# Performance work log

Measured on AMD Instinct MI355X. Metric: run time of the kernel, lower is better.

## Reference

```python
import jax, jax.numpy as jnp
import numpy as np

B, T, D, H = 2, 2048, 1024, 16
DH = D // H

def setup_inputs() -> dict:
    key = jax.random.key(0)
    ks = jax.random.split(key, 5)
    scale = 1.0 / np.sqrt(D)
    x = jax.random.normal(ks[0], (B, T, D), dtype=jnp.float32)
    Wq = jax.random.normal(ks[1], (D, D), dtype=jnp.float32) * scale
    Wk = jax.random.normal(ks[2], (D, D), dtype=jnp.float32) * scale
    Wv = jax.random.normal(ks[3], (D, D), dtype=jnp.float32) * scale
    Wo = jax.random.normal(ks[4], (D, D), dtype=jnp.float32) * scale
    # causal mask: True means masked (matches torch masked_fill semantics)
    mask = jnp.triu(jnp.ones((T, T), dtype=bool), k=1)
    return {"x": x, "mask": mask, "Wq": Wq, "Wk": Wk, "Wv": Wv, "Wo": Wo}

def reference(x, mask, Wq, Wk, Wv, Wo):
    b, t, c = x.shape
    # projections -> [B, H, T, DH]
    def split_heads(y):
        return y.reshape(b, t, H, DH).transpose(0, 2, 1, 3)
    q = split_heads(x @ Wq)
    k = split_heads(x @ Wk)
    v = split_heads(x @ Wv)
    # scores [B, H, T, T]
    att = jnp.einsum('bhqd,bhkd->bhqk', q, k) / jnp.sqrt(jnp.float32(DH))
    att = jnp.where(mask, -jnp.inf, att)
    att = jax.nn.softmax(att, axis=-1)
    # dropout=0.0 (eval-mode determinism)
    out = jnp.einsum('bhqk,bhkd->bhqd', att, v)
    out = out.transpose(0, 2, 1, 3).reshape(b, t, c)
    return out @ Wo
```

## Files before the change

kernel.cpp:

```cpp
#include <hip/hip_runtime.h>
#include <stdint.h>

typedef unsigned short u16;
typedef unsigned int u32;
typedef __attribute__((ext_vector_type(8))) short s16x8;
typedef __attribute__((ext_vector_type(4))) float f32x4;
typedef __attribute__((ext_vector_type(8))) unsigned short u16x8;
typedef __attribute__((ext_vector_type(4))) unsigned short u16x4;

#define T_ 2048
#define D_ 1024
#define H_ 16
#define DH_ 64

#define QSCALE_LOG2E 0.18033688011112042f

#if __has_builtin(__builtin_amdgcn_exp2f)
#define EXP2(x) __builtin_amdgcn_exp2f(x)
#else
#define EXP2(x) exp2f(x)
#endif

__device__ __forceinline__ float bf2f(u16 u) {
    union { unsigned int i; float f; } x; x.i = ((unsigned int)u) << 16; return x.f;
}
__device__ __forceinline__ u16 f2bf(float f) {
    union { float f; unsigned int i; } x; x.f = f;
    unsigned int u = x.i;
    u += 0x7fffu + ((u >> 16) & 1u);
    return (u16)(u >> 16);
}
__device__ __forceinline__ u32 pack_rn(float a, float b) {
    union { float f; u32 u; } ua, ub; ua.f = a; ub.f = b;
    return ((ua.u + 0x8000u) >> 16) | ((ub.u + 0x8000u) & 0xffff0000u);
}
__device__ __forceinline__ u32 cvtpk(float lo, float hi) {
    u32 r;
    asm("v_cvt_pk_bf16_f32 %0, %1, %2" : "=v"(r) : "v"(lo), "v"(hi));
    return r;
}
__device__ __forceinline__ void plswap32(u32 &a, u32 &b) {
    asm("v_permlane32_swap_b32 %0, %1" : "+v"(a), "+v"(b));
}
__device__ __forceinline__ void plswap16(u32 &a, u32 &b) {
    asm("v_permlane16_swap_b32 %0, %1" : "+v"(a), "+v"(b));
}
__device__ __forceinline__ s16x8 frag4(u32 a, u32 b, u32 c, u32 d) {
    union { u32 u[4]; s16x8 v; } x;
    x.u[0] = a; x.u[1] = b; x.u[2] = c; x.u[3] = d; return x.v;
}
__device__ __forceinline__ void p_frags(const f32x4 s[4], s16x8 &p0, s16x8 &p1) {
    u32 w00 = cvtpk(s[0][0], s[0][1]), w01 = cvtpk(s[0][2], s[0][3]);
    u32 w10 = cvtpk(s[1][0], s[1][1]), w11 = cvtpk(s[1][2], s[1][3]);
    u32 w20 = cvtpk(s[2][0], s[2][1]), w21 = cvtpk(s[2][2], s[2][3]);
    u32 w30 = cvtpk(s[3][0], s[3][1]), w31 = cvtpk(s[3][2], s[3][3]);
    plswap32(w00, w10); plswap16(w00, w10);
    plswap32(w01, w11); plswap16(w01, w11);
    plswap32(w20, w30); plswap16(w20, w30);
    plswap32(w21, w31); plswap16(w21, w31);
    p0 = frag4(w00, w01, w10, w11);
    p1 = frag4(w20, w21, w30, w31);
}

__device__ __forceinline__ void gload16(const u16* g, u16* l) {
    __builtin_amdgcn_global_load_lds(
        (const __attribute__((address_space(1))) void*)g,
        (__attribute__((address_space(3))) void*)l,
        16, 0, 0);
}

__global__ __launch_bounds__(256) void prep_kernel(const float* __restrict__ x,
                                                   const float* __restrict__ Wq,
                                                   const float* __restrict__ Wk,
                                                   const float* __restrict__ Wv,
                                                   const float* __restrict__ Wo,
                                                   u16* __restrict__ xb,
                                                   u16* __restrict__ WT) {
    __shared__ float tile[32][33];
    int blk = blockIdx.x;
    if (blk < 4096) {
        int i = (blk * 256 + threadIdx.x) * 4;
        float4 v = *(const float4*)(x + i);
        u16x4 o;
        o[0] = f2bf(v.x); o[1] = f2bf(v.y); o[2] = f2bf(v.z); o[3] = f2bf(v.w);
        *(u16x4*)(xb + i) = o;
    } else {
        int t = blk - 4096;
        int s = t >> 10;
        const float* W = (s == 0) ? Wq : (s == 1) ? Wk : (s == 2) ? Wv : Wo;
        int n0 = ((t >> 5) & 31) * 32;
        int k0 = (t & 31) * 32;
        int tx = threadIdx.x & 31, ty = threadIdx.x >> 5;
        #pragma unroll
        for (int j = 0; j < 32; j += 8)
            tile[ty + j][tx] = W[(k0 + ty + j) * D_ + n0 + tx];
        __syncthreads();
        u16* dst = WT + (size_t)s * D_ * D_;
        #pragma unroll
        for (int j = 0; j < 32; j += 8)
            dst[(n0 + ty + j) * D_ + k0 + tx] = f2bf(tile[tx][ty + j]);
    }
}

__global__ __launch_bounds__(256) void gemm_qkv(const u16* __restrict__ A,
                                                const u16* __restrict__ Bt,
                                                u16* __restrict__ Qw,
                                                u16* __restrict__ Kw,
                                                u16* __restrict__ Vw) {
    __shared__ __align__(16) u16 As[2][128 * 32];
    __shared__ __align__(16) u16 Bs[2][128 * 32];
    const int m0 = blockIdx.x * 128, n0 = blockIdx.y * 128;
    int tid = threadIdx.x;
    int w = tid >> 6, lane = tid & 63, quad = lane >> 4, l15 = lane & 15;
    int wr = w >> 1, wc = w & 1;

    int nb0 = (w << 7), nb1 = nb0 + 64;
    int c0 = nb0 + lane, c1 = nb1 + lane;
    int r0 = c0 >> 2, k0off = (((c0 & 3) ^ ((r0 >> 1) & 3)) << 3);
    int r1 = c1 >> 2, k1off = (((c1 & 3) ^ ((r1 >> 1) & 3)) << 3);
    const u16* Ar0 = A + (size_t)(m0 + r0) * D_ + k0off;
    const u16* Ar1 = A + (size_t)(m0 + r1) * D_ + k1off;
    const u16* Br0 = Bt + (size_t)(n0 + r0) * D_ + k0off;
    const u16* Br1 = Bt + (size_t)(n0 + r1) * D_ + k1off;

    f32x4 acc[4][4];
    #pragma unroll
    for (int mi = 0; mi < 4; ++mi)
        #pragma unroll
        for (int ni = 0; ni < 4; ++ni) acc[mi][ni] = (f32x4){0.f, 0.f, 0.f, 0.f};

    gload16(Ar0, &As[0][nb0 << 3]);
    gload16(Ar1, &As[0][nb1 << 3]);
    gload16(Br0, &Bs[0][nb0 << 3]);
    gload16(Br1, &Bs[0][nb1 << 3]);

    for (int k0 = 0; k0 < D_; k0 += 32) {
        int buf = (k0 >> 5) & 1;
        __syncthreads();
        if (k0 + 32 < D_) {
            int kn = k0 + 32;
            gload16(Ar0 + kn, &As[buf ^ 1][nb0 << 3]);
            gload16(Ar1 + kn, &As[buf ^ 1][nb1 << 3]);
            gload16(Br0 + kn, &Bs[buf ^ 1][nb0 << 3]);
            gload16(Br1 + kn, &Bs[buf ^ 1][nb1 << 3]);
        }
        s16x8 af[4], bf[4];
        #pragma unroll
        for (int mi = 0; mi < 4; ++mi) {
            int R = wr * 64 + mi * 16 + l15;
            af[mi] = *(const s16x8*)&As[buf][((R << 2) | (quad ^ ((R >> 1) & 3))) << 3];
        }
        #pragma unroll
        for (int ni = 0; ni < 4; ++ni) {
            int R = wc * 64 + ni * 16 + l15;
            bf[ni] = *(const s16x8*)&Bs[buf][((R << 2) | (quad ^ ((R >> 1) & 3))) << 3];
        }
        #pragma unroll
        for (int mi = 0; mi < 4; ++mi)
            #pragma unroll
            for (int ni = 0; ni < 4; ++ni)
                acc[mi][ni] = __builtin_amdgcn_mfma_f32_16x16x32_bf16(af[mi], bf[ni],
                                                                      acc[mi][ni], 0, 0, 0);
    }

    #pragma unroll
    for (int mi = 0; mi < 4; ++mi) {
        int mbase = m0 + wr * 64 + mi * 16 + quad * 4;
        #pragma unroll
        for (int ni = 0; ni < 4; ++ni) {
            int n = n0 + wc * 64 + ni * 16 + l15;
            int b = mbase >> 11, t0 = mbase & 2047;
            int sel = n >> 10, nn = n & 1023;
            int h = nn >> 6, dh = nn & 63;
            int bhidx = (b << 4) + h;
            if (sel == 0) {
                #pragma unroll
                for (int r = 0; r < 4; ++r)
                    Qw[(size_t)(bhidx * T_ + t0 + r) * DH_ + dh] =
                        f2bf(acc[mi][ni][r] * QSCALE_LOG2E);
            } else if (sel == 1) {
                #pragma unroll
                for (int r = 0; r < 4; ++r)
                    Kw[(size_t)(bhidx * T_ + t0 + r) * DH_ + dh] = f2bf(acc[mi][ni][r]);
            } else {
                uint2 pk;
                pk.x = pack_rn(acc[mi][ni][0], acc[mi][ni][1]);
                pk.y = pack_rn(acc[mi][ni][2], acc[mi][ni][3]);
                *(uint2*)(Vw + ((size_t)bhidx * DH_ + dh) * T_ + t0) = pk;
            }
        }
    }
}

__global__ __launch_bounds__(256) void gemm_out(const u16* __restrict__ A,
                                                const u16* __restrict__ Bt,
                                                float* __restrict__ Cout) {
    __shared__ __align__(16) u16 As[2][128 * 32];
    __shared__ __align__(16) u16 Bs[2][128 * 32];
    const int m0 = blockIdx.x * 128, n0 = blockIdx.y * 128;
    int tid = threadIdx.x;
    int w = tid >> 6, lane = tid & 63, quad = lane >> 4, l15 = lane & 15;
    int wr = w >> 1, wc = w & 1;

    int nb0 = (w << 7), nb1 = nb0 + 64;
    int c0 = nb0 + lane, c1 = nb1 + lane;
    int r0 = c0 >> 2, k0off = (((c0 & 3) ^ ((r0 >> 1) & 3)) << 3);
    int r1 = c1 >> 2, k1off = (((c1 & 3) ^ ((r1 >> 1) & 3)) << 3);
    const u16* Ar0 = A + (size_t)(m0 + r0) * D_ + k0off;
    const u16* Ar1 = A + (size_t)(m0 + r1) * D_ + k1off;
    const u16* Br0 = Bt + (size_t)(n0 + r0) * D_ + k0off;
    const u16* Br1 = Bt + (size_t)(n0 + r1) * D_ + k1off;

    f32x4 acc[4][4];
    #pragma unroll
    for (int mi = 0; mi < 4; ++mi)
        #pragma unroll
        for (int ni = 0; ni < 4; ++ni) acc[mi][ni] = (f32x4){0.f, 0.f, 0.f, 0.f};

    gload16(Ar0, &As[0][nb0 << 3]);
    gload16(Ar1, &As[0][nb1 << 3]);
    gload16(Br0, &Bs[0][nb0 << 3]);
    gload16(Br1, &Bs[0][nb1 << 3]);

    for (int k0 = 0; k0 < D_; k0 += 32) {
        int buf = (k0 >> 5) & 1;
        __syncthreads();
        if (k0 + 32 < D_) {
            int kn = k0 + 32;
            gload16(Ar0 + kn, &As[buf ^ 1][nb0 << 3]);
            gload16(Ar1 + kn, &As[buf ^ 1][nb1 << 3]);
            gload16(Br0 + kn, &Bs[buf ^ 1][nb0 << 3]);
            gload16(Br1 + kn, &Bs[buf ^ 1][nb1 << 3]);
        }
        s16x8 af[4], bf[4];
        #pragma unroll
        for (int mi = 0; mi < 4; ++mi) {
            int R = wr * 64 + mi * 16 + l15;
            af[mi] = *(const s16x8*)&As[buf][((R << 2) | (quad ^ ((R >> 1) & 3))) << 3];
        }
        #pragma unroll
        for (int ni = 0; ni < 4; ++ni) {
            int R = wc * 64 + ni * 16 + l15;
            bf[ni] = *(const s16x8*)&Bs[buf][((R << 2) | (quad ^ ((R >> 1) & 3))) << 3];
        }
        #pragma unroll
        for (int mi = 0; mi < 4; ++mi)
            #pragma unroll
            for (int ni = 0; ni < 4; ++ni)
                acc[mi][ni] = __builtin_amdgcn_mfma_f32_16x16x32_bf16(af[mi], bf[ni],
                                                                      acc[mi][ni], 0, 0, 0);
    }

    #pragma unroll
    for (int mi = 0; mi < 4; ++mi) {
        int mbase = m0 + wr * 64 + mi * 16 + quad * 4;
        #pragma unroll
        for (int ni = 0; ni < 4; ++ni) {
            int n = n0 + wc * 64 + ni * 16 + l15;
            #pragma unroll
            for (int r = 0; r < 4; ++r)
                Cout[(size_t)(mbase + r) * D_ + n] = acc[mi][ni][r];
        }
    }
}

__global__ __launch_bounds__(256, 4) void attn_mfma_kernel(const u16* __restrict__ Qg,
                                                           const u16* __restrict__ Kg,
                                                           const u16* __restrict__ Vt,
                                                           u16* __restrict__ Opart,
                                                           float* __restrict__ lpart) {
    __shared__ __align__(16) u16 Kbuf[2][64 * 64];
    __shared__ __align__(16) u16 Vbuf[2][64 * 64];

    int blk = blockIdx.x;
    int xcd = blk & 7, slot = blk >> 3;
    int bh = (xcd << 2) + (slot / 40);
    int x  = slot % 40;
    int BX, c;
    if (x < 4)       { BX = x;                    c = 0; }
    else if (x < 12) { BX = 4 + ((x - 4) >> 1);   c = (x - 4) & 1; }
    else if (x < 24) { BX = 8 + (x - 12) / 3;     c = (x - 12) % 3; }
    else             { BX = 12 + ((x - 24) >> 2); c = (x - 24) & 3; }
    int ktm = 2 * BX + 1;
    int ntile = ktm + 1;
    int nch = (BX >> 2) + 1;
    int base = ntile / nch, rem = ntile % nch;
    int kstart = c * base + (c < rem ? c : rem);
    int kend = kstart + base + (c < rem ? 1 : 0);

    int tid = threadIdx.x;
    int w = tid >> 6, lane = tid & 63, quad = lane >> 4, l15 = lane & 15;
    int q0 = BX << 7;
    int qA = q0 + 16 * w;
    int qB = q0 + 64 + 16 * w;

    const u16* Qb = Qg + (size_t)bh * T_ * DH_;
    const u16* Kb = Kg + (size_t)bh * T_ * DH_;
    const u16* Vb = Vt + (size_t)bh * DH_ * T_;

    s16x8 qa0 = *(const s16x8*)(Qb + (size_t)(qA + l15) * DH_ + quad * 8);
    s16x8 qa1 = *(const s16x8*)(Qb + (size_t)(qA + l15) * DH_ + quad * 8 + 32);
    s16x8 qc0 = *(const s16x8*)(Qb + (size_t)(qB + l15) * DH_ + quad * 8);
    s16x8 qc1 = *(const s16x8*)(Qb + (size_t)(qB + l15) * DH_ + quad * 8 + 32);

    int nb0 = (w << 7), nb1 = nb0 + 64;
    int n0c = nb0 + lane, n1c = nb1 + lane;
    int r0 = n0c >> 3, c0s = n0c & 7, g0 = (r0 << 3) + (c0s ^ (r0 & 7));
    int r1 = n1c >> 3, c1s = n1c & 7, g1 = (r1 << 3) + (c1s ^ (r1 & 7));

    {
        int kb0 = kstart << 6;
        const u16* Ktile = Kb + (size_t)kb0 * DH_;
        gload16(Ktile + (g0 << 3), &Kbuf[0][nb0 << 3]);
        gload16(Ktile + (g1 << 3), &Kbuf[0][nb1 << 3]);
        gload16(Vb + (size_t)r0 * T_ + kb0 + ((g0 & 7) << 3), &Vbuf[0][nb0 << 3]);
        gload16(Vb + (size_t)r1 * T_ + kb0 + ((g1 & 7) << 3), &Vbuf[0][nb1 << 3]);
    }

    f32x4 oA[4] = {{0.f,0.f,0.f,0.f},{0.f,0.f,0.f,0.f},{0.f,0.f,0.f,0.f},{0.f,0.f,0.f,0.f}};
    f32x4 oB[4] = {{0.f,0.f,0.f,0.f},{0.f,0.f,0.f,0.f},{0.f,0.f,0.f,0.f},{0.f,0.f,0.f,0.f}};
    float lA = 0.f, lB = 0.f;
    float lA1 = 0.f, lB1 = 0.f;

    for (int kt = kstart; kt < kend; ++kt) {
        int buf = (kt - kstart) & 1;
        __syncthreads();

        if (kt + 1 < kend) {
            int kb2 = (kt + 1) << 6;
            const u16* Ktile = Kb + (size_t)kb2 * DH_;
            gload16(Ktile + (g0 << 3), &Kbuf[buf ^ 1][nb0 << 3]);
            gload16(Ktile + (g1 << 3), &Kbuf[buf ^ 1][nb1 << 3]);
            gload16(Vb + (size_t)r0 * T_ + kb2 + ((g0 & 7) << 3), &Vbuf[buf ^ 1][nb0 << 3]);
            gload16(Vb + (size_t)r1 * T_ + kb2 + ((g1 & 7) << 3), &Vbuf[buf ^ 1][nb1 << 3]);
        }

        const bool liveA = (kt < ktm);

        f32x4 sA[4], sB[4];
        #pragma unroll
        for (int g = 0; g < 4; ++g) {
            int r = (g << 4) + l15;
            int cc = quad ^ (r & 7);
            s16x8 ka0 = *(const s16x8*)&Kbuf[buf][((r << 3) + cc) << 3];
            s16x8 ka1 = *(const s16x8*)&Kbuf[buf][((r << 3) + (cc ^ 4)) << 3];
            f32x4 z = {0.f, 0.f, 0.f, 0.f};
            sB[g] = __builtin_amdgcn_mfma_f32_16x16x32_bf16(ka0, qc0, z, 0, 0, 0);
            sB[g] = __builtin_amdgcn_mfma_f32_16x16x32_bf16(ka1, qc1, sB[g], 0, 0, 0);
            if (liveA) {
                sA[g] = __builtin_amdgcn_mfma_f32_16x16x32_bf16(ka0, qa0, z, 0, 0, 0);
                sA[g] = __builtin_amdgcn_mfma_f32_16x16x32_bf16(ka1, qa1, sA[g], 0, 0, 0);
            }
        }

        if (liveA && kt == ktm - 1) {
            int rA = 16 * w + l15;
            #pragma unroll
            for (int g = 0; g < 4; ++g)
                #pragma unroll
                for (int r = 0; r < 4; ++r)
                    if ((g << 4) + (quad << 2) + r > rA) sA[g][r] = -INFINITY;
        }
        if (kt == ktm) {
            int rB = 16 * w + l15;
            #pragma unroll
            for (int g = 0; g < 4; ++g)
                #pragma unroll
                for (int r = 0; r < 4; ++r)
                    if ((g << 4) + (quad << 2) + r > rB) sB[g][r] = -INFINITY;
        }

        #pragma unroll
        for (int g = 0; g < 4; ++g) {
            float pB0 = EXP2(sB[g][0]); sB[g][0] = pB0; lB  += pB0;
            float pB1 = EXP2(sB[g][1]); sB[g][1] = pB1; lB1 += pB1;
            float pB2 = EXP2(sB[g][2]); sB[g][2] = pB2; lB  += pB2;
            float pB3 = EXP2(sB[g][3]); sB[g][3] = pB3; lB1 += pB3;
        }
        if (liveA) {
            #pragma unroll
            for (int g = 0; g < 4; ++g) {
                float pA0 = EXP2(sA[g][0]); sA[g][0] = pA0; lA  += pA0;
                float pA1 = EXP2(sA[g][1]); sA[g][1] = pA1; lA1 += pA1;
                float pA2 = EXP2(sA[g][2]); sA[g][2] = pA2; lA  += pA2;
                float pA3 = EXP2(sA[g][3]); sA[g][3] = pA3; lA1 += pA3;
            }
        }

        s16x8 pa0, pa1, pc0, pc1;
        p_frags(sB, pc0, pc1);
        if (liveA) p_frags(sA, pa0, pa1);

        #pragma unroll
        for (int g = 0; g < 4; ++g) {
            int r = (g << 4) + l15;
            int cc = quad ^ (r & 7);
            s16x8 va0 = *(const s16x8*)&Vbuf[buf][((r << 3) + cc) << 3];
            s16x8 va1 = *(const s16x8*)&Vbuf[buf][((r << 3) + (cc ^ 4)) << 3];
            oB[g] = __builtin_amdgcn_mfma_f32_16x16x32_bf16(va0, pc0, oB[g], 0, 0, 0);
            oB[g] = __builtin_amdgcn_mfma_f32_16x16x32_bf16(va1, pc1, oB[g], 0, 0, 0);
            if (liveA) {
                oA[g] = __builtin_amdgcn_mfma_f32_16x16x32_bf16(va0, pa0, oA[g], 0, 0, 0);
                oA[g] = __builtin_amdgcn_mfma_f32_16x16x32_bf16(va1, pa1, oA[g], 0, 0, 0);
            }
        }
    }

    lA += lA1; lB += lB1;
    lA += __shfl_xor(lA, 16); lA += __shfl_xor(lA, 32);
    lB += __shfl_xor(lB, 16); lB += __shfl_xor(lB, 32);
    int slotid = ((bh << 4) + BX) * 4 + c;
    u16* dA = Opart + ((size_t)slotid * 128 + 16 * w + l15) * 64;
    u16* dB = dA + 64 * 64;
    #pragma unroll
    for (int g = 0; g < 4; ++g) {
        uint2 pk;
        pk.x = cvtpk(oA[g][0], oA[g][1]); pk.y = cvtpk(oA[g][2], oA[g][3]);
        *(uint2*)(dA + (g << 4) + (quad << 2)) = pk;
        pk.x = cvtpk(oB[g][0], oB[g][1]); pk.y = cvtpk(oB[g][2], oB[g][3]);
        *(uint2*)(dB + (g << 4) + (quad << 2)) = pk;
    }
    if (quad == 0) {
        lpart[(size_t)slotid * 128 + 16 * w + l15] = lA;
        lpart[(size_t)slotid * 128 + 64 + 16 * w + l15] = lB;
    }
}

__global__ __launch_bounds__(256) void reduce_attn(const u16* __restrict__ Opart,
                                                   const float* __restrict__ lpart,
                                                   u16* __restrict__ att) {
    int BX = blockIdx.x, bh = blockIdx.y;
    int nch = (BX >> 2) + 1;
    int tid = threadIdx.x;
    int row = tid >> 1, dh0 = (tid & 1) << 5;
    int slotbase = ((bh << 4) + BX) << 2;

    float acc[32];
    #pragma unroll
    for (int i = 0; i < 32; ++i) acc[i] = 0.f;
    float l = 0.f;
    for (int cc = 0; cc < nch; ++cc) {
        const u16* op = Opart + ((size_t)(slotbase + cc) * 128 + row) * 64 + dh0;
        #pragma unroll
        for (int v = 0; v < 4; ++v) {
            u16x8 o8 = *(const u16x8*)(op + v * 8);
            #pragma unroll
            for (int j = 0; j < 8; ++j) acc[v * 8 + j] += bf2f(o8[j]);
        }
        l += lpart[(size_t)(slotbase + cc) * 128 + row];
    }
    float inv = 1.f / l;
    int b = bh >> 4, h = bh & 15;
    int q = (BX << 7) + row;
    u16* dst = att + ((size_t)(b * T_) + q) * D_ + (h << 6) + dh0;
    #pragma unroll
    for (int v = 0; v < 4; ++v) {
        u16x8 o8;
        #pragma unroll
        for (int j = 0; j < 8; ++j) o8[j] = f2bf(acc[v * 8 + j] * inv);
        *(u16x8*)(dst + v * 8) = o8;
    }
}

extern "C" void kernel_launch(void* const* d_in, const int* in_sizes, int n_in,
                              void* d_out, int out_size, void* d_ws, size_t ws_size,
                              hipStream_t stream) {
    const float* x  = (const float*)d_in[0];
    const float* Wq = (const float*)d_in[2];
    const float* Wk = (const float*)d_in[3];
    const float* Wv = (const float*)d_in[4];
    const float* Wo = (const float*)d_in[5];
    float* out = (float*)d_out;

    char* ws = (char*)d_ws;
    u16*   xb    = (u16*)(ws);
    u16*   WT    = (u16*)(ws + (8ull  << 20));
    u16*   Qw    = (u16*)(ws + (16ull << 20));
    u16*   Kw    = (u16*)(ws + (24ull << 20));
    u16*   Vw    = (u16*)(ws + (32ull << 20));
    u16*   att   = (u16*)(ws + (40ull << 20));
    u16*   Opart = (u16*)(ws + (48ull << 20));
    float* lpart = (float*)(ws + (82ull << 20));

    prep_kernel<<<dim3(8192), dim3(256), 0, stream>>>(x, Wq, Wk, Wv, Wo, xb, WT);
    gemm_qkv<<<dim3(32, 24), dim3(256), 0, stream>>>(xb, WT, Qw, Kw, Vw);
    attn_mfma_kernel<<<dim3(1280), dim3(256), 0, stream>>>(Qw, Kw, Vw, Opart, lpart);
    reduce_attn<<<dim3(16, 32), dim3(256), 0, stream>>>(Opart, lpart, att);
    gemm_out<<<dim3(32, 8), dim3(256), 0, stream>>>(att, WT + 3ull * 1048576ull, out);
}
```

Before: 187.8 us.

## Rewrite QKV GEMM as 256x256 tile, 8-wave pipelined kernel with interleaved loads

The QKV projection GEMM now computes a 256x256 output tile with 512 threads and a 64-wide K step. Global-to-LDS loads are split into quarter stages and interleaved with MFMA groups under explicit barriers, vmcnt waits and s_setprio, in a ping-pong schedule. The grid shrinks from 768 to 192 blocks. The goal is more data reuse per block and better overlap of memory traffic with matrix math, at the cost of much higher register and LDS use (128 KB LDS per block with launch bounds asking for 2 blocks per CU) and fewer blocks to spread across the CUs.

Measured after the change: 190.5 us. No clear change (+1.4%).

```diff
diff --git a/kernel.cpp b/kernel.cpp
--- a/kernel.cpp
+++ b/kernel.cpp
@@ -102,74 +102,140 @@
     }
 }
 
-__global__ __launch_bounds__(256) void gemm_qkv(const u16* __restrict__ A,
-                                                const u16* __restrict__ Bt,
-                                                u16* __restrict__ Qw,
-                                                u16* __restrict__ Kw,
-                                                u16* __restrict__ Vw) {
-    __shared__ __align__(16) u16 As[2][128 * 32];
-    __shared__ __align__(16) u16 Bs[2][128 * 32];
-    const int m0 = blockIdx.x * 128, n0 = blockIdx.y * 128;
+__global__ __launch_bounds__(512, 2) void gemm_qkv(const u16* __restrict__ A,
+                                                   const u16* __restrict__ Bt,
+                                                   u16* __restrict__ Qw,
+                                                   u16* __restrict__ Kw,
+                                                   u16* __restrict__ Vw) {
+    __shared__ __align__(16) u16 L[2][4][128 * 64];
+    const int m0 = blockIdx.x * 256, n0 = blockIdx.y * 256;
     int tid = threadIdx.x;
-    int w = tid >> 6, lane = tid & 63, quad = lane >> 4, l15 = lane & 15;
-    int wr = w >> 1, wc = w & 1;
-
-    int nb0 = (w << 7), nb1 = nb0 + 64;
-    int c0 = nb0 + lane, c1 = nb1 + lane;
-    int r0 = c0 >> 2, k0off = (((c0 & 3) ^ ((r0 >> 1) & 3)) << 3);
-    int r1 = c1 >> 2, k1off = (((c1 & 3) ^ ((r1 >> 1) & 3)) << 3);
-    const u16* Ar0 = A + (size_t)(m0 + r0) * D_ + k0off;
-    const u16* Ar1 = A + (size_t)(m0 + r1) * D_ + k1off;
-    const u16* Br0 = Bt + (size_t)(n0 + r0) * D_ + k0off;
-    const u16* Br1 = Bt + (size_t)(n0 + r1) * D_ + k1off;
-
-    f32x4 acc[4][4];
-    #pragma unroll
-    for (int mi = 0; mi < 4; ++mi)
-        #pragma unroll
-        for (int ni = 0; ni < 4; ++ni) acc[mi][ni] = (f32x4){0.f, 0.f, 0.f, 0.f};
-
-    gload16(Ar0, &As[0][nb0 << 3]);
-    gload16(Ar1, &As[0][nb1 << 3]);
-    gload16(Br0, &Bs[0][nb0 << 3]);
-    gload16(Br1, &Bs[0][nb1 << 3]);
-
-    for (int k0 = 0; k0 < D_; k0 += 32) {
-        int buf = (k0 >> 5) & 1;
-        __syncthreads();
-        if (k0 + 32 < D_) {
-            int kn = k0 + 32;
-            gload16(Ar0 + kn, &As[buf ^ 1][nb0 << 3]);
-            gload16(Ar1 + kn, &As[buf ^ 1][nb1 << 3]);
-            gload16(Br0 + kn, &Bs[buf ^ 1][nb0 << 3]);
-            gload16(Br1 + kn, &Bs[buf ^ 1][nb1 << 3]);
-        }
-        s16x8 af[4], bf[4];
-        #pragma unroll
-        for (int mi = 0; mi < 4; ++mi) {
-            int R = wr * 64 + mi * 16 + l15;
-            af[mi] = *(const s16x8*)&As[buf][((R << 2) | (quad ^ ((R >> 1) & 3))) << 3];
-        }
-        #pragma unroll
-        for (int ni = 0; ni < 4; ++ni) {
-            int R = wc * 64 + ni * 16 + l15;
-            bf[ni] = *(const s16x8*)&Bs[buf][((R << 2) | (quad ^ ((R >> 1) & 3))) << 3];
-        }
-        #pragma unroll
-        for (int mi = 0; mi < 4; ++mi)
-            #pragma unroll
-            for (int ni = 0; ni < 4; ++ni)
-                acc[mi][ni] = __builtin_amdgcn_mfma_f32_16x16x32_bf16(af[mi], bf[ni],
-                                                                      acc[mi][ni], 0, 0, 0);
-    }
-
-    #pragma unroll
-    for (int mi = 0; mi < 4; ++mi) {
-        int mbase = m0 + wr * 64 + mi * 16 + quad * 4;
+    int wid = tid >> 6, lane = tid & 63, quad = lane >> 4, l15 = lane & 15;
+    int wr = wid >> 2, wc = wid & 3;
+    int lswz = l15 & 7;
+    int cof0 = (quad ^ lswz) << 3;
+    int cof1 = ((4 | quad) ^ lswz) << 3;
+
+    int rl0 = (wid << 4) + (lane >> 3);
+    int ch = (lane & 7) ^ (rl0 & 7);
+    const u16* Asrc = A + (size_t)(m0 + rl0) * D_ + (ch << 3);
+    const u16* Bsrc = Bt + (size_t)(n0 + rl0) * D_ + (ch << 3);
+    int wbase = wid << 10;
+
+#define STG(kt, ab, h) do { \
+    int kk_ = (kt) < 16 ? (kt) : 15; \
+    const u16* s_ = ((ab) ? Bsrc : Asrc) + (size_t)(h) * (128 * D_) + (kk_ << 6); \
+    u16* d_ = &L[(kt) & 1][(ab) * 2 + (h)][wbase]; \
+    gload16(s_, d_); \
+    gload16(s_ + (D_ << 3), d_ + 512); \
+} while (0)
+
+#define LDA4(BUF, MI0) do { \
+    _Pragma("unroll") \
+    for (int mi_ = 0; mi_ < 4; ++mi_) { \
+        const u16* p_ = &L[BUF][wr][(((MI0) + mi_) * 16 + l15) * 64]; \
+        af[mi_][0] = *(const s16x8*)(p_ + cof0); \
+        af[mi_][1] = *(const s16x8*)(p_ + cof1); \
+    } \
+} while (0)
+
+#define LDB4(BUF, NI0, BB) do { \
+    _Pragma("unroll") \
+    for (int ni_ = 0; ni_ < 2; ++ni_) { \
+        const u16* p_ = &L[BUF][2 + (wc >> 1)][((wc & 1) * 64 + ((NI0) + ni_) * 16 + l15) * 64]; \
+        BB[ni_][0] = *(const s16x8*)(p_ + cof0); \
+        BB[ni_][1] = *(const s16x8*)(p_ + cof1); \
+    } \
+} while (0)
+
+#define MFMA16(MI0, NI0, BB) do { \
+    __builtin_amdgcn_s_setprio(1); \
+    _Pragma("unroll") \
+    for (int mi_ = 0; mi_ < 4; ++mi_) { \
+        _Pragma("unroll") \
+        for (int ni_ = 0; ni_ < 2; ++ni_) { \
+            acc[(MI0) + mi_][(NI0) + ni_] = __builtin_amdgcn_mfma_f32_16x16x32_bf16( \
+                af[mi_][0], BB[ni_][0], acc[(MI0) + mi_][(NI0) + ni_], 0, 0, 0); \
+            acc[(MI0) + mi_][(NI0) + ni_] = __builtin_amdgcn_mfma_f32_16x16x32_bf16( \
+                af[mi_][1], BB[ni_][1], acc[(MI0) + mi_][(NI0) + ni_], 0, 0, 0); \
+        } \
+    } \
+    __builtin_amdgcn_s_setprio(0); \
+} while (0)
+
+#define BAR() asm volatile("s_barrier" ::: "memory")
+#define WV4() asm volatile("s_waitcnt vmcnt(4)" ::: "memory")
+
+    s16x8 af[4][2], bb0[2][2], bb1[2][2];
+    f32x4 acc[8][4];
+    #pragma unroll
+    for (int i = 0; i < 8; ++i)
+        #pragma unroll
+        for (int j = 0; j < 4; ++j) acc[i][j] = (f32x4){0.f, 0.f, 0.f, 0.f};
+
+    STG(0, 0, 0); STG(0, 0, 1); STG(0, 1, 0); STG(0, 1, 1);
+    STG(1, 1, 0); STG(1, 1, 1);
+    WV4();
+    BAR();
+
+    for (int t = 0; t < 8; ++t) {
+        int k1 = 2 * t + 1, k2 = 2 * t + 2, k3 = 2 * t + 3;
+        LDA4(0, 0); LDB4(0, 0, bb0);
+        STG(k1, 0, 0);
+        BAR();
+        MFMA16(0, 0, bb0);
+        BAR();
+        LDB4(0, 2, bb1);
+        STG(k1, 0, 1);
+        BAR();
+        MFMA16(0, 2, bb1);
+        BAR();
+        LDA4(0, 4);
+        STG(k2, 1, 0);
+        BAR();
+        MFMA16(4, 0, bb0);
+        BAR();
+        STG(k2, 1, 1);
+        BAR();
+        MFMA16(4, 2, bb1);
+        WV4();
+        BAR();
+        LDA4(1, 0); LDB4(1, 0, bb0);
+        STG(k2, 0, 0);
+        BAR();
+        MFMA16(0, 0, bb0);
+        BAR();
+        LDB4(1, 2, bb1);
+        STG(k2, 0, 1);
+        BAR();
+        MFMA16(0, 2, bb1);
+        BAR();
+        LDA4(1, 4);
+        STG(k3, 1, 0);
+        BAR();
+        MFMA16(4, 0, bb0);
+        BAR();
+        STG(k3, 1, 1);
+        BAR();
+        MFMA16(4, 2, bb1);
+        WV4();
+        BAR();
+    }
+
+#undef STG
+#undef LDA4
+#undef LDB4
+#undef MFMA16
+#undef BAR
+#undef WV4
+
+    #pragma unroll
+    for (int mi = 0; mi < 8; ++mi) {
+        int mbase = m0 + wr * 128 + mi * 16 + quad * 4;
+        int b = mbase >> 11, t0 = mbase & 2047;
         #pragma unroll
         for (int ni = 0; ni < 4; ++ni) {
             int n = n0 + wc * 64 + ni * 16 + l15;
-            int b = mbase >> 11, t0 = mbase & 2047;
             int sel = n >> 10, nn = n & 1023;
             int h = nn >> 6, dh = nn & 63;
             int bhidx = (b << 4) + h;
@@ -483,7 +549,7 @@
     float* lpart = (float*)(ws + (82ull << 20));
 
     prep_kernel<<<dim3(8192), dim3(256), 0, stream>>>(x, Wq, Wk, Wv, Wo, xb, WT);
-    gemm_qkv<<<dim3(32, 24), dim3(256), 0, stream>>>(xb, WT, Qw, Kw, Vw);
+    gemm_qkv<<<dim3(16, 12), dim3(512), 0, stream>>>(xb, WT, Qw, Kw, Vw);
     attn_mfma_kernel<<<dim3(1280), dim3(256), 0, stream>>>(Qw, Kw, Vw, Opart, lpart);
     reduce_attn<<<dim3(16, 32), dim3(256), 0, stream>>>(Opart, lpart, att);
     gemm_out<<<dim3(32, 8), dim3(256), 0, stream>>>(att, WT + 3ull * 1048576ull, out);
```
